# Kernel tuning notes

Measured on AMD Instinct MI355X. Metric: run time of the kernel, lower is better.

## Reference

```python
import jax, jax.numpy as jnp
import numpy as np

BLOCK = 8      # block_size
HALO = 3       # halo_size
WIN = BLOCK + 2 * HALO   # 14, kv window size
NH = 8         # num_heads
DH = 32        # dim_head
DIM = 256
DIM_QK = NH * DH          # 256
DV = 256                  # dim_v = dim_out
DVH = DV // NH            # 32
SCALE = DH ** -0.5
REL = 2 * WIN - 1         # 27


def rel_logits_1d(q, rel_k, permute_mask):
    # q: (B, H, W, d); rel_k: (rel_size, d)
    B, H, W, d = q.shape
    rel_size = rel_k.shape[0]
    win = (rel_size + 1) // 2
    x = jnp.einsum('bhwd,rd->bhwr', q, rel_k).reshape(-1, W, rel_size)
    # skew trick: pad + reshape turns absolute into relative indexing
    x = jnp.pad(x, ((0, 0), (0, 0), (0, 1))).reshape(x.shape[0], -1)
    x = jnp.pad(x, ((0, 0), (0, rel_size - W))).reshape(-1, W + 1, rel_size)
    x = x[:, :W, win - 1:]
    x = jnp.broadcast_to(x.reshape(B, H, 1, W, win), (B, H, win, W, win))
    return jnp.transpose(x, permute_mask)


def pos_embed_rel(q, height_rel, width_rel):
    # q: (B*NH, num_blocks, block*block, DH)
    B, BB, HW, dh = q.shape
    q4 = q.reshape(-1, BLOCK, BLOCK, dh)
    rel_w = rel_logits_1d(q4, width_rel, (0, 1, 3, 2, 4))
    rel_h = rel_logits_1d(jnp.transpose(q4, (0, 2, 1, 3)), height_rel, (0, 3, 1, 4, 2))
    return (rel_h + rel_w).reshape(B, BB, HW, -1)


def setup_inputs() -> dict:
    key = jax.random.key(0)
    k1, k2, k3, k4, k5 = jax.random.split(key, 5)
    B, H, W = 4, 128, 128
    std = DIM ** -0.5
    return {
        'x': jax.random.normal(k1, (B, DIM, H, W), dtype=jnp.float32),
        'w_q': jax.random.normal(k2, (DIM_QK, DIM), dtype=jnp.float32) * std,
        'w_kv': jax.random.normal(k3, (DIM_QK + DV, DIM), dtype=jnp.float32) * std,
        'height_rel': jax.random.normal(k4, (REL, DH), dtype=jnp.float32) * SCALE,
        'width_rel': jax.random.normal(k5, (REL, DH), dtype=jnp.float32) * SCALE,
    }


def reference(x, w_q, w_kv, height_rel, width_rel):
    B, C, H, W = x.shape
    nhb, nwb = H // BLOCK, W // BLOCK
    nb = nhb * nwb
    # 1x1 convs as matmuls over channel dim
    q = jnp.einsum('bchw,oc->bohw', x, w_q)
    q = q.reshape(B * NH, DH, nhb, BLOCK, nwb, BLOCK)
    q = jnp.transpose(q, (0, 1, 3, 5, 2, 4)).reshape(B * NH, DH, BLOCK * BLOCK, nb)
    q = jnp.transpose(q, (0, 3, 2, 1))              # (B*NH, nb, bs^2, DH)

    kv = jnp.einsum('bchw,oc->bohw', x, w_kv)
    kv = jnp.pad(kv, ((0, 0), (0, 0), (HALO, HALO), (HALO, HALO)))
    ih = jnp.arange(nhb)[:, None] * BLOCK + jnp.arange(WIN)[None, :]
    iw = jnp.arange(nwb)[:, None] * BLOCK + jnp.arange(WIN)[None, :]
    kv = kv[:, :, ih]
    kv = kv[:, :, :, :, iw]
    kv = jnp.transpose(kv, (0, 1, 2, 4, 3, 5))
    kv = kv.reshape(B * NH, DH + DVH, nb, WIN * WIN)
    kv = jnp.transpose(kv, (0, 2, 3, 1))
    k, v = kv[..., :DH], kv[..., DH:]

    logits = jnp.einsum('bnqd,bnkd->bnqk', q, k) * SCALE
    logits = logits + pos_embed_rel(q, height_rel, width_rel)
    attn = jax.nn.softmax(logits, axis=-1)
    out = jnp.einsum('bnqk,bnkd->bnqd', attn, v)    # (B*NH, nb, bs^2, DVH)
    out = jnp.transpose(out, (0, 3, 2, 1))          # (B*NH, DVH, bs^2, nb)
    out = out.reshape(-1, BLOCK, BLOCK, nhb, nwb)
    out = jnp.transpose(out, (0, 3, 1, 4, 2)).reshape(B, DV, H, W)
    return out
```

## Files before the change

kernel.cpp:

```cpp
#include <hip/hip_runtime.h>
#include <stdint.h>


typedef short bf16s;
typedef bf16s bf16x8 __attribute__((ext_vector_type(8)));
typedef bf16s bf16x4 __attribute__((ext_vector_type(4)));
typedef float f32x4  __attribute__((ext_vector_type(4)));
typedef unsigned int u32x4 __attribute__((ext_vector_type(4)));

#define MFMA16(a, b, c) __builtin_amdgcn_mfma_f32_16x16x32_bf16(a, b, c, 0, 0, 0)
#define SCALE_QK 0.17677669529663687f
#define LOG2E 1.4426950408889634f
#define EXP_SHIFT 11.541560327111707f
#define SCLOG 0.25503486142f

__device__ __forceinline__ f32x4 pv_mfma(bf16x4 a, bf16x4 b, f32x4 c) {
#if __has_builtin(__builtin_amdgcn_mfma_f32_16x16x16bf16_1k)
  return __builtin_amdgcn_mfma_f32_16x16x16bf16_1k(a, b, c, 0, 0, 0);
#elif __has_builtin(__builtin_amdgcn_mfma_f32_16x16x16_bf16)
  return __builtin_amdgcn_mfma_f32_16x16x16_bf16(a, b, c, 0, 0, 0);
#else
  f32x4 d;
  asm volatile("v_mfma_f32_16x16x16_bf16 %0, %1, %2, %3\n\ts_nop 4\n\ts_nop 4"
               : "=v"(d) : "v"(a), "v"(b), "v"(c));
  return d;
#endif
}

__device__ __forceinline__ void async16(void* lds, const void* g) {
  __builtin_amdgcn_global_load_lds(
      (const __attribute__((address_space(1))) unsigned int*)g,
      (__attribute__((address_space(3))) unsigned int*)lds, 16, 0, 0);
}

__device__ __forceinline__ bf16s f2b(float f) {
  unsigned int u = __builtin_bit_cast(unsigned int, f);
  u = (u + 0x7fffu + ((u >> 16) & 1u)) >> 16;
  return (bf16s)u;
}

__global__ __launch_bounds__(256) void k_convert(const float* __restrict__ wq,
                                                 const float* __restrict__ wkv,
                                                 const float* __restrict__ hrel,
                                                 const float* __restrict__ wrel,
                                                 bf16s* __restrict__ wq_b,
                                                 bf16s* __restrict__ wkv_b,
                                                 bf16s* __restrict__ rel_b) {
  int i = blockIdx.x * 256 + threadIdx.x;
  if (i < 65536) {
    wq_b[i] = f2b(wq[i]);
  } else if (i < 196608) {
    int j = i - 65536;
    wkv_b[j] = f2b(wkv[j]);
  } else {
    int r2 = i - 196608;
    int relid = r2 >> 10, r = (r2 >> 5) & 31, d = r2 & 31;
    const float* src = relid ? hrel : wrel;
    rel_b[r2] = (r < 27) ? f2b(src[r * 32 + d]) : (bf16s)0;
  }
}

__global__ __launch_bounds__(256) void k_transpose(const float* __restrict__ x,
                                                   bf16s* __restrict__ xT) {
  __shared__ bf16s tile[64][72];
  const int ct = blockIdx.x, pt = blockIdx.y, b = blockIdx.z;
  const int t = threadIdx.x;
  const int r0 = t >> 3, c8 = (t & 7) * 8;
  const float* src = x + ((size_t)b * 256 + ct * 64) * 16384 + (size_t)pt * 64;
#pragma unroll
  for (int pass = 0; pass < 2; ++pass) {
    int r = pass * 32 + r0;
    const float4* sp = (const float4*)(src + (size_t)r * 16384 + c8);
    float4 f0 = sp[0], f1 = sp[1];
    bf16x8 v;
    v[0] = f2b(f0.x); v[1] = f2b(f0.y); v[2] = f2b(f0.z); v[3] = f2b(f0.w);
    v[4] = f2b(f1.x); v[5] = f2b(f1.y); v[6] = f2b(f1.z); v[7] = f2b(f1.w);
    *(bf16x8*)&tile[r][c8] = v;
  }
  __syncthreads();
  bf16s* dst = xT + ((size_t)b * 16384 + pt * 64) * 256 + ct * 64;
#pragma unroll
  for (int pass = 0; pass < 2; ++pass) {
    int p = pass * 32 + r0;
    bf16x8 v;
#pragma unroll
    for (int u = 0; u < 8; ++u) v[u] = tile[c8 + u][p];
    *(bf16x8*)(dst + (size_t)p * 256 + c8) = v;
  }
}

__global__ __launch_bounds__(256) void k_zero_border(bf16s* __restrict__ kv) {
  const int gid = blockIdx.x * 256 + threadIdx.x;
  const int chunk = gid & 63;
  const int rest = gid >> 6;
  const int b = rest / 1572, pxi = rest % 1572;
  int y, x;
  if (pxi < 804) {
    int r = pxi / 134;
    x = pxi % 134;
    y = (r < 3) ? r : 128 + r;
  } else {
    int p2 = pxi - 804;
    y = 3 + p2 / 6;
    int xi = p2 % 6;
    x = (xi < 3) ? xi : 128 + xi;
  }
  u32x4 z = {0, 0, 0, 0};
  *(u32x4*)(kv + (((size_t)b * 134 + y) * 134 + x) * 512 + chunk * 8) = z;
}

__global__ __launch_bounds__(256) void k_qkv(const bf16s* __restrict__ wq,
                                             const bf16s* __restrict__ wkv,
                                             const bf16s* __restrict__ xT,
                                             bf16s* __restrict__ q_ws,
                                             bf16s* __restrict__ kv_ws) {
  __shared__ __align__(16) bf16s smem[17408];
  const int wgid = blockIdx.x;
  const int xcd = wgid & 7, ii = wgid >> 3;
  const int mt = ii % 6;
  const int p = xcd * 64 + ii / 6;
  const int y = p >> 2, b = p & 3;
  const int t = threadIdx.x;
  const int wv = t >> 6, lane = t & 63, g = lane >> 4, l15 = lane & 15;
  const int wm = wv & 1, wn = wv >> 1;
  const bf16s* Ag = (mt < 2) ? (wq + mt * 128 * 256) : (wkv + (mt - 2) * 128 * 256);
  const bf16s* Bg = xT + ((size_t)b * 16384 + y * 128) * 256;

  f32x4 acc[4][4];
#pragma unroll
  for (int i = 0; i < 4; ++i)
#pragma unroll
    for (int j = 0; j < 4; ++j) acc[i][j] = (f32x4){0.f, 0.f, 0.f, 0.f};

  const int s_row = ((unsigned)t) >> 2;
  const int s_k8 = (t & 3) * 8;
#define STAGE(kc_, cur_)                                                      \
  do {                                                                        \
    _Pragma("unroll")                                                         \
    for (int hh = 0; hh < 2; ++hh) {                                          \
      int row = hh * 64 + s_row;                                              \
      async16((char*)smem + (cur_)*16384 + hh * 4096 + wv * 1024,             \
              Ag + row * 256 + (kc_)*32 + s_k8);                              \
      async16((char*)smem + 8192 + (cur_)*16384 + hh * 4096 + wv * 1024,      \
              Bg + row * 256 + (kc_)*32 + s_k8);                              \
    }                                                                         \
  } while (0)

  STAGE(0, 0);
  __syncthreads();
  int cur = 0;
#pragma unroll
  for (int kc = 0; kc < 8; ++kc) {
    if (kc < 7) STAGE(kc + 1, cur ^ 1);
    const bf16s* Alc = (const bf16s*)((char*)smem + cur * 16384);
    const bf16s* Blc = (const bf16s*)((char*)smem + 8192 + cur * 16384);
    bf16x8 af[4], bfr[4];
#pragma unroll
    for (int mi = 0; mi < 4; ++mi)
      af[mi] = *(const bf16x8*)&Alc[(wm * 64 + mi * 16 + l15) * 32 + g * 8];
#pragma unroll
    for (int ni = 0; ni < 4; ++ni)
      bfr[ni] = *(const bf16x8*)&Blc[(wn * 64 + ni * 16 + l15) * 32 + g * 8];
#pragma unroll
    for (int mi = 0; mi < 4; ++mi)
#pragma unroll
      for (int ni = 0; ni < 4; ++ni)
        acc[mi][ni] = MFMA16(af[mi], bfr[ni], acc[mi][ni]);
    __syncthreads();
    cur ^= 1;
  }
#undef STAGE

  bf16s* Cl = smem;
#pragma unroll
  for (int mi = 0; mi < 4; ++mi)
#pragma unroll
    for (int ni = 0; ni < 4; ++ni)
#pragma unroll
      for (int rg = 0; rg < 4; ++rg) {
        int m = wm * 64 + mi * 16 + g * 4 + rg;
        int n = wn * 64 + ni * 16 + l15;
        Cl[n * 136 + m] = f2b(acc[mi][ni][rg]);
      }
  __syncthreads();

  if (mt < 2) {
#pragma unroll
    for (int hh = 0; hh < 2; ++hh) {
      int rid = hh * 256 + t;
      int head = rid >> 7, bx = (rid >> 3) & 15, wc = rid & 7;
      int px = bx * 8 + wc;
      bf16s* dst = q_ws +
          ((((size_t)(b * 8 + mt * 4 + head) * 256 + (y >> 3) * 16 + bx) * 64 +
            (y & 7) * 8 + wc)) * 32;
#pragma unroll
      for (int c4 = 0; c4 < 4; ++c4)
        *(bf16x8*)(dst + c4 * 8) = *(const bf16x8*)&Cl[px * 136 + head * 32 + c4 * 8];
    }
  } else {
    int px = t >> 1, half = t & 1;
    bf16s* dst = kv_ws + (((size_t)b * 134 + y + 3) * 134 + px + 3) * 512 +
                 (mt - 2) * 128 + half * 64;
#pragma unroll
    for (int c8 = 0; c8 < 8; ++c8)
      *(bf16x8*)(dst + c8 * 8) = *(const bf16x8*)&Cl[px * 136 + half * 64 + c8 * 8];
  }
}

#define VSTRIDE 228
__global__ __launch_bounds__(256, 5) void k_attn(const bf16s* __restrict__ q_ws,
                                                 const bf16s* __restrict__ kv_ws,
                                                 const bf16s* __restrict__ rel_b,
                                                 float* __restrict__ outp) {
  __shared__ __align__(16) char arena[32000];
  bf16s* vT = (bf16s*)arena;
  const int t = threadIdx.x;
  const int wv = t >> 6, lane = t & 63, g = lane >> 4, l15 = lane & 15;
  char* pw = arena + 14592 + wv * 4352;
  float* RWp = (float*)pw;
  float* RHp = RWp + 544;

  int wgid = blockIdx.x;
  int xcd = wgid & 7, chnk = wgid >> 3;
  int bxlo = chnk & 3, rest = chnk >> 2;
  int c = xcd * 256 + rest;
  int bx = (c & 3) * 4 + bxlo;
  int byy = (c >> 2) & 15;
  int bh = c >> 6;
  int b = bh >> 3, hd = bh & 7;
  int blk = byy * 16 + bx;

  const bf16s* kvb = kv_ws + (((size_t)b * 134 + byy * 8) * 134 + bx * 8) * 512 + hd * 64;
  const bf16s* qg  = q_ws + ((size_t)bh * 256 + blk) * 2048;

  bf16x8 aq = *(const bf16x8*)(qg + (wv * 16 + l15) * 32 + g * 8);
  const int i_cl = (l15 < 14) ? l15 : 13;
  const bf16s* kbase = kvb + (size_t)i_cl * 68608 + g * 8;
  bf16x8 kf[14];
#pragma unroll
  for (int nt = 0; nt < 14; ++nt)
    kf[nt] = *(const bf16x8*)(kbase + nt * 512);
  bf16x8 wf[2], hf[2];
#pragma unroll
  for (int t16 = 0; t16 < 2; ++t16) {
    wf[t16] = *(const bf16x8*)(rel_b + (t16 * 16 + l15) * 32 + g * 8);
    hf[t16] = *(const bf16x8*)(rel_b + 1024 + (t16 * 16 + l15) * 32 + g * 8);
  }

  for (int idx = t; idx < 784; idx += 256) {
    int pos = idx >> 2, ch = idx & 3;
    int i = pos / 14, j = pos - i * 14;
    bf16x8 v = *(const bf16x8*)(kvb + (size_t)(i * 134 + j) * 512 + 32 + ch * 8);
#pragma unroll
    for (int u = 0; u < 8; ++u) vT[(ch * 8 + u) * VSTRIDE + j * 16 + i] = v[u];
  }
  for (int idx = t; idx < 896; idx += 256) {
    int d = idx / 28, r = idx - d * 28;
    vT[d * VSTRIDE + (r >> 1) * 16 + 14 + (r & 1)] = 0;
  }

  f32x4 acc[14];
#pragma unroll
  for (int nt = 0; nt < 14; ++nt) acc[nt] = (f32x4){0.f, 0.f, 0.f, 0.f};
#pragma unroll
  for (int nt = 0; nt < 14; ++nt) acc[nt] = MFMA16(kf[nt], aq, acc[nt]);

  {
    f32x4 zz = (f32x4){0.f, 0.f, 0.f, 0.f};
#pragma unroll
    for (int t16 = 0; t16 < 2; ++t16) {
      f32x4 rw = MFMA16(wf[t16], aq, zz);
      f32x4 rh = MFMA16(hf[t16], aq, zz);
      float* wd = &RWp[l15 * 34 + t16 * 16 + g * 4];
      float* hd2 = &RHp[l15 * 34 + t16 * 16 + g * 4];
      *(float2*)wd       = make_float2(fmaf(rw[0], LOG2E, -EXP_SHIFT),
                                       fmaf(rw[1], LOG2E, -EXP_SHIFT));
      *(float2*)(wd + 2) = make_float2(fmaf(rw[2], LOG2E, -EXP_SHIFT),
                                       fmaf(rw[3], LOG2E, -EXP_SHIFT));
      *(float2*)hd2       = make_float2(rh[0] * LOG2E, rh[1] * LOG2E);
      *(float2*)(hd2 + 2) = make_float2(rh[2] * LOG2E, rh[3] * LOG2E);
    }
  }

  const int jq = l15 & 7;
  const int iq = wv * 2 + (l15 >> 3);
  const float* RWr = RWp + l15 * 34;
  const float* RHr = RHp + l15 * 34;
  const int ihb = 13 + g * 4 - iq;
  float h0 = RHr[ihb], h1 = RHr[ihb + 1], h2 = RHr[ihb + 2], h3 = RHr[ihb + 3];
  float sm = 0.f;
#pragma unroll
  for (int nt = 0; nt < 14; ++nt) {
    float w1 = RWr[13 + nt - jq];
    float e0 = exp2f(fmaf(acc[nt][0], SCLOG, w1 + h0));
    float e1 = exp2f(fmaf(acc[nt][1], SCLOG, w1 + h1));
    float e2 = exp2f(fmaf(acc[nt][2], SCLOG, w1 + h2));
    float e3 = exp2f(fmaf(acc[nt][3], SCLOG, w1 + h3));
    if (g == 3) { e2 = 0.f; e3 = 0.f; }
    sm += e0 + e1 + e2 + e3;
    acc[nt][0] = e0; acc[nt][1] = e1; acc[nt][2] = e2; acc[nt][3] = e3;
  }
  sm += __shfl_xor(sm, 16);
  sm += __shfl_xor(sm, 32);
  float rs = __builtin_amdgcn_rcpf(sm);

  __syncthreads();

  f32x4 oa0 = (f32x4){0.f, 0.f, 0.f, 0.f};
  f32x4 oa1 = (f32x4){0.f, 0.f, 0.f, 0.f};
#pragma unroll
  for (int nt = 0; nt < 14; ++nt) {
    bf16x4 bpv;
    bpv[0] = f2b(acc[nt][0]); bpv[1] = f2b(acc[nt][1]);
    bpv[2] = f2b(acc[nt][2]); bpv[3] = f2b(acc[nt][3]);
    bf16x4 a0 = *(const bf16x4*)(vT + l15 * VSTRIDE + nt * 16 + g * 4);
    bf16x4 a1 = *(const bf16x4*)(vT + (16 + l15) * VSTRIDE + nt * 16 + g * 4);
    oa0 = pv_mfma(a0, bpv, oa0);
    oa1 = pv_mfma(a1, bpv, oa1);
  }

  {
    int py = wv * 2 + (l15 >> 3), px = l15 & 7;
    float* ob = outp + (((size_t)(b * 256 + hd * 32) * 128 + byy * 8 + py) * 128) +
                bx * 8 + px;
#pragma unroll
    for (int rg = 0; rg < 4; ++rg) {
      ob[(size_t)(g * 4 + rg) * 16384] = oa0[rg] * rs;
      ob[(size_t)(16 + g * 4 + rg) * 16384] = oa1[rg] * rs;
    }
  }
}

extern "C" void kernel_launch(void* const* d_in, const int* in_sizes, int n_in,
                              void* d_out, int out_size, void* d_ws, size_t ws_size,
                              hipStream_t stream) {
  (void)in_sizes; (void)n_in; (void)out_size; (void)ws_size;
  const float* x    = (const float*)d_in[0];
  const float* wq   = (const float*)d_in[1];
  const float* wkv  = (const float*)d_in[2];
  const float* hrel = (const float*)d_in[3];
  const float* wrel = (const float*)d_in[4];
  float* outp = (float*)d_out;

  bf16s* xT    = (bf16s*)d_ws;
  bf16s* q_ws  = xT + 16777216;
  bf16s* kv_ws = q_ws + 16777216;
  bf16s* wq_b  = kv_ws + 36773888;
  bf16s* wkv_b = wq_b + 65536;
  bf16s* rel_b = wkv_b + 131072;

  hipLaunchKernelGGL(k_convert,    dim3(776),       dim3(256), 0, stream,
                     wq, wkv, hrel, wrel, wq_b, wkv_b, rel_b);
  hipLaunchKernelGGL(k_transpose,  dim3(4, 256, 4), dim3(256), 0, stream, x, xT);
  hipLaunchKernelGGL(k_zero_border, dim3(1572),     dim3(256), 0, stream, kv_ws);
  hipLaunchKernelGGL(k_qkv,        dim3(3072),      dim3(256), 0, stream,
                     wq_b, wkv_b, xT, q_ws, kv_ws);
  hipLaunchKernelGGL(k_attn,       dim3(8192),      dim3(256), 0, stream,
                     q_ws, kv_ws, rel_b, outp);
}
```

Measured before the change: 268.5 us.

## Fuse input transpose and bf16 conversion into QKV GEMM B-operand staging

Removes the separate transpose kernel that wrote a bf16 channel-last copy of x. The QKV GEMM now loads fp32 x directly with strided float2 reads, converts to bf16 in registers and writes a padded LDS tile, with register prefetch overlapping the MFMA work. This saves a kernel launch and a full intermediate write/read, but each tile re-reads fp32 input (twice the bytes) with strided access across channels.

```diff
diff --git a/kernel.cpp b/kernel.cpp
--- a/kernel.cpp
+++ b/kernel.cpp
@@ -60,35 +60,6 @@
   }
 }
 
-__global__ __launch_bounds__(256) void k_transpose(const float* __restrict__ x,
-                                                   bf16s* __restrict__ xT) {
-  __shared__ bf16s tile[64][72];
-  const int ct = blockIdx.x, pt = blockIdx.y, b = blockIdx.z;
-  const int t = threadIdx.x;
-  const int r0 = t >> 3, c8 = (t & 7) * 8;
-  const float* src = x + ((size_t)b * 256 + ct * 64) * 16384 + (size_t)pt * 64;
-#pragma unroll
-  for (int pass = 0; pass < 2; ++pass) {
-    int r = pass * 32 + r0;
-    const float4* sp = (const float4*)(src + (size_t)r * 16384 + c8);
-    float4 f0 = sp[0], f1 = sp[1];
-    bf16x8 v;
-    v[0] = f2b(f0.x); v[1] = f2b(f0.y); v[2] = f2b(f0.z); v[3] = f2b(f0.w);
-    v[4] = f2b(f1.x); v[5] = f2b(f1.y); v[6] = f2b(f1.z); v[7] = f2b(f1.w);
-    *(bf16x8*)&tile[r][c8] = v;
-  }
-  __syncthreads();
-  bf16s* dst = xT + ((size_t)b * 16384 + pt * 64) * 256 + ct * 64;
-#pragma unroll
-  for (int pass = 0; pass < 2; ++pass) {
-    int p = pass * 32 + r0;
-    bf16x8 v;
-#pragma unroll
-    for (int u = 0; u < 8; ++u) v[u] = tile[c8 + u][p];
-    *(bf16x8*)(dst + (size_t)p * 256 + c8) = v;
-  }
-}
-
 __global__ __launch_bounds__(256) void k_zero_border(bf16s* __restrict__ kv) {
   const int gid = blockIdx.x * 256 + threadIdx.x;
   const int chunk = gid & 63;
@@ -111,7 +82,7 @@
 
 __global__ __launch_bounds__(256) void k_qkv(const bf16s* __restrict__ wq,
                                              const bf16s* __restrict__ wkv,
-                                             const bf16s* __restrict__ xT,
+                                             const float* __restrict__ x,
                                              bf16s* __restrict__ q_ws,
                                              bf16s* __restrict__ kv_ws) {
   __shared__ __align__(16) bf16s smem[17408];
@@ -124,7 +95,6 @@
   const int wv = t >> 6, lane = t & 63, g = lane >> 4, l15 = lane & 15;
   const int wm = wv & 1, wn = wv >> 1;
   const bf16s* Ag = (mt < 2) ? (wq + mt * 128 * 256) : (wkv + (mt - 2) * 128 * 256);
-  const bf16s* Bg = xT + ((size_t)b * 16384 + y * 128) * 256;
 
   f32x4 acc[4][4];
 #pragma unroll
@@ -132,44 +102,73 @@
 #pragma unroll
     for (int j = 0; j < 4; ++j) acc[i][j] = (f32x4){0.f, 0.f, 0.f, 0.f};
 
-  const int s_row = ((unsigned)t) >> 2;
+  const int s_row = t >> 2;
   const int s_k8 = (t & 3) * 8;
-#define STAGE(kc_, cur_)                                                      \
+#define ASTAGE(kc_, cur_)                                                     \
   do {                                                                        \
     _Pragma("unroll")                                                         \
     for (int hh = 0; hh < 2; ++hh) {                                          \
       int row = hh * 64 + s_row;                                              \
-      async16((char*)smem + (cur_)*16384 + hh * 4096 + wv * 1024,             \
+      async16((char*)smem + (cur_)*8192 + hh * 4096 + wv * 1024,              \
               Ag + row * 256 + (kc_)*32 + s_k8);                              \
-      async16((char*)smem + 8192 + (cur_)*16384 + hh * 4096 + wv * 1024,      \
-              Bg + row * 256 + (kc_)*32 + s_k8);                              \
     }                                                                         \
   } while (0)
 
-  STAGE(0, 0);
+  const int px0 = (t >> 2) * 2;
+  const int k0 = (t & 3) * 8;
+  const float* xsrc = x + (size_t)b * 4194304 + (size_t)y * 128 + px0;
+#define BLOAD(kc_, xv_)                                                       \
+  do {                                                                        \
+    _Pragma("unroll")                                                         \
+    for (int u = 0; u < 8; ++u)                                               \
+      xv_[u] = *(const float2*)(xsrc + (size_t)((kc_)*32 + k0 + u) * 16384);  \
+  } while (0)
+#define BWRITE(cur_, xv_)                                                     \
+  do {                                                                        \
+    bf16x8 w0, w1;                                                            \
+    _Pragma("unroll")                                                         \
+    for (int u = 0; u < 8; ++u) { w0[u] = f2b(xv_[u].x); w1[u] = f2b(xv_[u].y); } \
+    bf16s* Bl_ = (bf16s*)((char*)smem + 16384 + (cur_)*9216);                 \
+    *(bf16x8*)&Bl_[px0 * 36 + k0] = w0;                                       \
+    *(bf16x8*)&Bl_[(px0 + 1) * 36 + k0] = w1;                                 \
+  } while (0)
+
+  {
+    float2 xv0[8];
+    BLOAD(0, xv0);
+    ASTAGE(0, 0);
+    BWRITE(0, xv0);
+  }
   __syncthreads();
   int cur = 0;
 #pragma unroll
   for (int kc = 0; kc < 8; ++kc) {
-    if (kc < 7) STAGE(kc + 1, cur ^ 1);
-    const bf16s* Alc = (const bf16s*)((char*)smem + cur * 16384);
-    const bf16s* Blc = (const bf16s*)((char*)smem + 8192 + cur * 16384);
+    float2 xn[8];
+    if (kc < 7) {
+      ASTAGE(kc + 1, cur ^ 1);
+      BLOAD(kc + 1, xn);
+    }
+    const bf16s* Alc = (const bf16s*)((char*)smem + cur * 8192);
+    const bf16s* Blc = (const bf16s*)((char*)smem + 16384 + cur * 9216);
     bf16x8 af[4], bfr[4];
 #pragma unroll
     for (int mi = 0; mi < 4; ++mi)
       af[mi] = *(const bf16x8*)&Alc[(wm * 64 + mi * 16 + l15) * 32 + g * 8];
 #pragma unroll
     for (int ni = 0; ni < 4; ++ni)
-      bfr[ni] = *(const bf16x8*)&Blc[(wn * 64 + ni * 16 + l15) * 32 + g * 8];
+      bfr[ni] = *(const bf16x8*)&Blc[(wn * 64 + ni * 16 + l15) * 36 + g * 8];
 #pragma unroll
     for (int mi = 0; mi < 4; ++mi)
 #pragma unroll
       for (int ni = 0; ni < 4; ++ni)
         acc[mi][ni] = MFMA16(af[mi], bfr[ni], acc[mi][ni]);
+    if (kc < 7) BWRITE(cur ^ 1, xn);
     __syncthreads();
     cur ^= 1;
   }
-#undef STAGE
+#undef ASTAGE
+#undef BLOAD
+#undef BWRITE
 
   bf16s* Cl = smem;
 #pragma unroll
@@ -351,10 +350,9 @@
 
   hipLaunchKernelGGL(k_convert,    dim3(776),       dim3(256), 0, stream,
                      wq, wkv, hrel, wrel, wq_b, wkv_b, rel_b);
-  hipLaunchKernelGGL(k_transpose,  dim3(4, 256, 4), dim3(256), 0, stream, x, xT);
   hipLaunchKernelGGL(k_zero_border, dim3(1572),     dim3(256), 0, stream, kv_ws);
   hipLaunchKernelGGL(k_qkv,        dim3(3072),      dim3(256), 0, stream,
-                     wq_b, wkv_b, xT, q_ws, kv_ws);
+                     wq_b, wkv_b, x, q_ws, kv_ws);
   hipLaunchKernelGGL(k_attn,       dim3(8192),      dim3(256), 0, stream,
                      q_ws, kv_ws, rel_b, outp);
 }
```

After: 305.1 us. 13.6% more time.
